# Kernel optimization log

Hardware: AMD Instinct MI355X
Metric: run time of the kernel (lower is better)

## Reference

```python
import jax, jax.numpy as jnp
import numpy as np

_JPEG_QUANT_TABLE = np.array([
    [16, 11, 10, 16, 24, 40, 51, 61],
    [12, 12, 14, 19, 26, 58, 60, 55],
    [14, 13, 16, 24, 40, 57, 69, 56],
    [14, 17, 22, 29, 51, 87, 80, 62],
    [18, 22, 37, 56, 68, 109, 103, 77],
    [24, 35, 55, 64, 81, 104, 113, 92],
    [49, 64, 78, 87, 103, 121, 120, 101],
    [72, 92, 95, 98, 112, 100, 103, 99]], dtype=np.float32)


def _dct_matrix():
    # Orthonormal 8x8 DCT-II basis: D[k, i] = alpha(k) * cos(pi*(2i+1)k/16)
    n = 8
    k = np.arange(n)[:, None].astype(np.float64)
    i = np.arange(n)[None, :].astype(np.float64)
    alpha = np.where(k == 0, np.sqrt(1.0 / n), np.sqrt(2.0 / n))
    return jnp.asarray(alpha * np.cos(np.pi * (2 * i + 1) * k / (2 * n)), dtype=jnp.float32)


def setup_inputs() -> dict:
    key = jax.random.key(0)
    image = jax.random.uniform(key, (32, 3, 512, 512), dtype=jnp.float32)
    return {"image": image, "quality": 75}


def reference(image, quality):
    B, C, H, W = image.shape  # H, W divisible by 8 (no padding branch needed)
    bh, bw = H // 8, W // 8

    # libjpeg quality -> scale (quality is a static Python int)
    scale = 5000.0 / quality if quality < 50 else 200.0 - 2.0 * quality
    qtable = jnp.clip(jnp.asarray(_JPEG_QUANT_TABLE) * scale / 100.0, 1.0, 255.0)
    dct = _dct_matrix()

    x = image - 0.5
    # blockify: (B,C,H,W) -> (B*C, bh, bw, 8, 8)
    blocks = x.reshape(B * C, bh, 8, bw, 8).transpose(0, 1, 3, 2, 4)

    # 2D DCT: dct @ block @ dct^T
    dct_blocks = jnp.einsum('ki,...ij,lj->...kl', dct, blocks, dct)

    # quantize with straight-through estimator (forward: round, backward: identity)
    normalized = dct_blocks / qtable
    quantized = normalized + jax.lax.stop_gradient(jnp.round(normalized) - normalized)
    dequantized = quantized * qtable

    # 2D IDCT: dct^T @ block @ dct
    spatial = jnp.einsum('ki,...kl,lj->...ij', dct, dequantized, dct)

    # deblockify: (B*C, bh, bw, 8, 8) -> (B, C, H, W)
    result = spatial.transpose(0, 1, 3, 2, 4).reshape(B, C, H, W)
    return jnp.clip(result + 0.5, 0.0, 1.0)
```

## Files before the change

### kernel.cpp

```cpp
#include <hip/hip_runtime.h>


typedef float v4f __attribute__((ext_vector_type(4)));

static __device__ __constant__ float c_qbase[64] = {
    16.f, 11.f, 10.f, 16.f, 24.f, 40.f, 51.f, 61.f,
    12.f, 12.f, 14.f, 19.f, 26.f, 58.f, 60.f, 55.f,
    14.f, 13.f, 16.f, 24.f, 40.f, 57.f, 69.f, 56.f,
    14.f, 17.f, 22.f, 29.f, 51.f, 87.f, 80.f, 62.f,
    18.f, 22.f, 37.f, 56.f, 68.f, 109.f, 103.f, 77.f,
    24.f, 35.f, 55.f, 64.f, 81.f, 104.f, 113.f, 92.f,
    49.f, 64.f, 78.f, 87.f, 103.f, 121.f, 120.f, 101.f,
    72.f, 92.f, 95.f, 98.f, 112.f, 100.f, 103.f, 99.f
};

#define LDS_PITCH 9

__global__ __launch_bounds__(256, 8)
void jpeg_row_kernel(const float* __restrict__ in, const int* __restrict__ qual,
                     float* __restrict__ out) {
    constexpr float CE[4][4] = {
        { 0.3535533906f,  0.3535533906f,  0.3535533906f,  0.3535533906f },
        { 0.4619397663f,  0.1913417162f, -0.1913417162f, -0.4619397663f },
        { 0.3535533906f, -0.3535533906f, -0.3535533906f,  0.3535533906f },
        { 0.1913417162f, -0.4619397663f,  0.4619397663f, -0.1913417162f }
    };
    constexpr float CO[4][4] = {
        { 0.4903926402f,  0.4157348062f,  0.2777851165f,  0.0975451610f },
        { 0.4157348062f, -0.0975451610f, -0.4903926402f, -0.2777851165f },
        { 0.2777851165f, -0.4903926402f,  0.0975451610f,  0.4157348062f },
        { 0.0975451610f, -0.2777851165f,  0.4157348062f, -0.4903926402f }
    };

    __shared__ float2 qlds[64];
    __shared__ float tr[256 * LDS_PITCH];

    const int tid = threadIdx.x;

    {
        int q = qual[0];
        double sd = (q < 50) ? (5000.0 / (double)q) : (200.0 - 2.0 * (double)q);
        float scale = (float)sd;
        int e = tid & 63;
        float v = c_qbase[e] * scale / 100.0f;
        v = fminf(fmaxf(v, 1.0f), 255.0f);
        qlds[e] = make_float2(v, 1.0f / v);
    }

    const int gt  = blockIdx.x * 256 + tid;
    const int b   = gt >> 3;
    const int r   = gt & 7;
    const int img = b >> 12;
    const int by  = (b >> 6) & 63;
    const int bx  = b & 63;
    const long rowaddr = (((long)img * 512 + (long)by * 8 + r) * 512) + (long)bx * 8;

    float x[8];
    {
        const float4 a  = *reinterpret_cast<const float4*>(in + rowaddr);
        const float4 b4 = *reinterpret_cast<const float4*>(in + rowaddr + 4);
        x[0] = a.x - 0.5f; x[1] = a.y - 0.5f; x[2] = a.z - 0.5f; x[3] = a.w - 0.5f;
        x[4] = b4.x - 0.5f; x[5] = b4.y - 0.5f; x[6] = b4.z - 0.5f; x[7] = b4.w - 0.5f;
    }

    float qk[8], rqk[8];
#pragma unroll
    for (int k = 0; k < 8; ++k) {
        float2 t2 = qlds[k * 8 + r];
        qk[k] = t2.x; rqk[k] = t2.y;
    }

    float u[8];
    {
        float e[4], o[4];
#pragma unroll
        for (int j = 0; j < 4; ++j) { e[j] = x[j] + x[7 - j]; o[j] = x[j] - x[7 - j]; }
#pragma unroll
        for (int m = 0; m < 4; ++m) {
            float se = 0.0f, so = 0.0f;
#pragma unroll
            for (int j = 0; j < 4; ++j) {
                se = fmaf(e[j], CE[m][j], se);
                so = fmaf(o[j], CO[m][j], so);
            }
            u[2 * m] = se; u[2 * m + 1] = so;
        }
    }

    const int base_w = tid * LDS_PITCH;
    const int base_r = (tid & ~7) * LDS_PITCH;
#pragma unroll
    for (int j = 0; j < 8; ++j) tr[base_w + j] = u[j];
    float t[8];
#pragma unroll
    for (int j = 0; j < 8; ++j) t[j] = tr[base_r + j * LDS_PITCH + r];

    float y[8];
    {
        float e[4], o[4];
#pragma unroll
        for (int j = 0; j < 4; ++j) { e[j] = t[j] + t[7 - j]; o[j] = t[j] - t[7 - j]; }
#pragma unroll
        for (int m = 0; m < 4; ++m) {
            float se = 0.0f, so = 0.0f;
#pragma unroll
            for (int j = 0; j < 4; ++j) {
                se = fmaf(e[j], CE[m][j], se);
                so = fmaf(o[j], CO[m][j], so);
            }
            y[2 * m]     = rintf(se * rqk[2 * m])     * qk[2 * m];
            y[2 * m + 1] = rintf(so * rqk[2 * m + 1]) * qk[2 * m + 1];
        }
    }

    float v[8];
#pragma unroll
    for (int j = 0; j < 4; ++j) {
        float a = 0.0f, bb = 0.0f;
#pragma unroll
        for (int m = 0; m < 4; ++m) {
            a  = fmaf(y[2 * m],     CE[m][j], a);
            bb = fmaf(y[2 * m + 1], CO[m][j], bb);
        }
        v[j] = a + bb; v[7 - j] = a - bb;
    }

#pragma unroll
    for (int j = 0; j < 8; ++j) tr[base_w + j] = v[j];
    float w[8];
#pragma unroll
    for (int j = 0; j < 8; ++j) w[j] = tr[base_r + j * LDS_PITCH + r];

    float srow[8];
#pragma unroll
    for (int j = 0; j < 4; ++j) {
        float a = 0.0f, bb = 0.0f;
#pragma unroll
        for (int m = 0; m < 4; ++m) {
            a  = fmaf(w[2 * m],     CE[m][j], a);
            bb = fmaf(w[2 * m + 1], CO[m][j], bb);
        }
        float s0 = a + bb + 0.5f;
        float s1 = a - bb + 0.5f;
        srow[j]     = fminf(fmaxf(s0, 0.0f), 1.0f);
        srow[7 - j] = fminf(fmaxf(s1, 0.0f), 1.0f);
    }
    *reinterpret_cast<float4*>(out + rowaddr)     = make_float4(srow[0], srow[1], srow[2], srow[3]);
    *reinterpret_cast<float4*>(out + rowaddr + 4) = make_float4(srow[4], srow[5], srow[6], srow[7]);
}

extern "C" void kernel_launch(void* const* d_in, const int* in_sizes, int n_in,
                              void* d_out, int out_size, void* d_ws, size_t ws_size,
                              hipStream_t stream) {
    const float* img  = (const float*)d_in[0];
    const int*   qual = (const int*)d_in[1];
    float*       out  = (float*)d_out;

    const int nthreads_total = (out_size / 64) * 8;
    const int block = 256;
    const int grid = nthreads_total / block;

    jpeg_row_kernel<<<grid, block, 0, stream>>>(img, qual, out);
}
```

Before: 38.69 us.

## Process six image planes per thread with register-prefetched loads

Each thread now loops over six 8-pixel rows spaced sixteen image planes apart, so the grid shrinks to a fixed 2048 blocks. The next row's global loads are issued before the current row's DCT/quantize/IDCT, overlapping memory latency with compute and amortizing the quant-table setup. LDS transpose writes are widened to 128-bit vector stores. The fixed grid and NITER hard-code the 96-plane 512x512 input shape, and the vector LDS stores at pitch 9 are only 4-byte aligned for odd thread indices.

```diff
diff --git a/kernel.cpp b/kernel.cpp
--- a/kernel.cpp
+++ b/kernel.cpp
@@ -15,10 +15,11 @@
 };
 
 #define LDS_PITCH 9
+#define NITER 6
 
 __global__ __launch_bounds__(256, 8)
-void jpeg_row_kernel(const float* __restrict__ in, const int* __restrict__ qual,
-                     float* __restrict__ out) {
+void jpeg_persist_kernel(const float* __restrict__ in, const int* __restrict__ qual,
+                         float* __restrict__ out) {
     constexpr float CE[4][4] = {
         { 0.3535533906f,  0.3535533906f,  0.3535533906f,  0.3535533906f },
         { 0.4619397663f,  0.1913417162f, -0.1913417162f, -0.4619397663f },
@@ -53,15 +54,8 @@
     const int img = b >> 12;
     const int by  = (b >> 6) & 63;
     const int bx  = b & 63;
-    const long rowaddr = (((long)img * 512 + (long)by * 8 + r) * 512) + (long)bx * 8;
-
-    float x[8];
-    {
-        const float4 a  = *reinterpret_cast<const float4*>(in + rowaddr);
-        const float4 b4 = *reinterpret_cast<const float4*>(in + rowaddr + 4);
-        x[0] = a.x - 0.5f; x[1] = a.y - 0.5f; x[2] = a.z - 0.5f; x[3] = a.w - 0.5f;
-        x[4] = b4.x - 0.5f; x[5] = b4.y - 0.5f; x[6] = b4.z - 0.5f; x[7] = b4.w - 0.5f;
-    }
+    long addr = (((long)img * 512 + (long)by * 8 + r) * 512) + (long)bx * 8;
+    const long step = 16L * 512 * 512;
 
     float qk[8], rqk[8];
 #pragma unroll
@@ -70,83 +64,100 @@
         qk[k] = t2.x; rqk[k] = t2.y;
     }
 
-    float u[8];
-    {
-        float e[4], o[4];
-#pragma unroll
-        for (int j = 0; j < 4; ++j) { e[j] = x[j] + x[7 - j]; o[j] = x[j] - x[7 - j]; }
-#pragma unroll
-        for (int m = 0; m < 4; ++m) {
-            float se = 0.0f, so = 0.0f;
-#pragma unroll
-            for (int j = 0; j < 4; ++j) {
-                se = fmaf(e[j], CE[m][j], se);
-                so = fmaf(o[j], CO[m][j], so);
-            }
-            u[2 * m] = se; u[2 * m + 1] = so;
-        }
-    }
-
     const int base_w = tid * LDS_PITCH;
     const int base_r = (tid & ~7) * LDS_PITCH;
-#pragma unroll
-    for (int j = 0; j < 8; ++j) tr[base_w + j] = u[j];
-    float t[8];
-#pragma unroll
-    for (int j = 0; j < 8; ++j) t[j] = tr[base_r + j * LDS_PITCH + r];
 
-    float y[8];
-    {
-        float e[4], o[4];
-#pragma unroll
-        for (int j = 0; j < 4; ++j) { e[j] = t[j] + t[7 - j]; o[j] = t[j] - t[7 - j]; }
-#pragma unroll
-        for (int m = 0; m < 4; ++m) {
-            float se = 0.0f, so = 0.0f;
-#pragma unroll
-            for (int j = 0; j < 4; ++j) {
-                se = fmaf(e[j], CE[m][j], se);
-                so = fmaf(o[j], CO[m][j], so);
-            }
-            y[2 * m]     = rintf(se * rqk[2 * m])     * qk[2 * m];
-            y[2 * m + 1] = rintf(so * rqk[2 * m + 1]) * qk[2 * m + 1];
-        }
-    }
-
-    float v[8];
-#pragma unroll
-    for (int j = 0; j < 4; ++j) {
-        float a = 0.0f, bb = 0.0f;
-#pragma unroll
-        for (int m = 0; m < 4; ++m) {
-            a  = fmaf(y[2 * m],     CE[m][j], a);
-            bb = fmaf(y[2 * m + 1], CO[m][j], bb);
-        }
-        v[j] = a + bb; v[7 - j] = a - bb;
-    }
+    float4 a  = *reinterpret_cast<const float4*>(in + addr);
+    float4 b4 = *reinterpret_cast<const float4*>(in + addr + 4);
 
 #pragma unroll
-    for (int j = 0; j < 8; ++j) tr[base_w + j] = v[j];
-    float w[8];
+    for (int it = 0; it < NITER; ++it) {
+        float x[8];
+        x[0] = a.x - 0.5f; x[1] = a.y - 0.5f; x[2] = a.z - 0.5f; x[3] = a.w - 0.5f;
+        x[4] = b4.x - 0.5f; x[5] = b4.y - 0.5f; x[6] = b4.z - 0.5f; x[7] = b4.w - 0.5f;
+        if (it + 1 < NITER) {
+            a  = *reinterpret_cast<const float4*>(in + addr + step);
+            b4 = *reinterpret_cast<const float4*>(in + addr + step + 4);
+        }
+
+        float u[8];
+        {
+            float e[4], o[4];
 #pragma unroll
-    for (int j = 0; j < 8; ++j) w[j] = tr[base_r + j * LDS_PITCH + r];
+            for (int j = 0; j < 4; ++j) { e[j] = x[j] + x[7 - j]; o[j] = x[j] - x[7 - j]; }
+#pragma unroll
+            for (int m = 0; m < 4; ++m) {
+                float se = 0.0f, so = 0.0f;
+#pragma unroll
+                for (int j = 0; j < 4; ++j) {
+                    se = fmaf(e[j], CE[m][j], se);
+                    so = fmaf(o[j], CO[m][j], so);
+                }
+                u[2 * m] = se; u[2 * m + 1] = so;
+            }
+        }
 
-    float srow[8];
+        *reinterpret_cast<v4f*>(&tr[base_w])     = *reinterpret_cast<v4f*>(&u[0]);
+        *reinterpret_cast<v4f*>(&tr[base_w + 4]) = *reinterpret_cast<v4f*>(&u[4]);
+        float t[8];
 #pragma unroll
-    for (int j = 0; j < 4; ++j) {
-        float a = 0.0f, bb = 0.0f;
+        for (int j = 0; j < 8; ++j) t[j] = tr[base_r + j * LDS_PITCH + r];
+
+        float y[8];
+        {
+            float e[4], o[4];
 #pragma unroll
-        for (int m = 0; m < 4; ++m) {
-            a  = fmaf(w[2 * m],     CE[m][j], a);
-            bb = fmaf(w[2 * m + 1], CO[m][j], bb);
+            for (int j = 0; j < 4; ++j) { e[j] = t[j] + t[7 - j]; o[j] = t[j] - t[7 - j]; }
+#pragma unroll
+            for (int m = 0; m < 4; ++m) {
+                float se = 0.0f, so = 0.0f;
+#pragma unroll
+                for (int j = 0; j < 4; ++j) {
+                    se = fmaf(e[j], CE[m][j], se);
+                    so = fmaf(o[j], CO[m][j], so);
+                }
+                y[2 * m]     = rintf(se * rqk[2 * m])     * qk[2 * m];
+                y[2 * m + 1] = rintf(so * rqk[2 * m + 1]) * qk[2 * m + 1];
+            }
         }
-        float s0 = a + bb + 0.5f;
-        float s1 = a - bb + 0.5f;
-        srow[j]     = fminf(fmaxf(s0, 0.0f), 1.0f);
-        srow[7 - j] = fminf(fmaxf(s1, 0.0f), 1.0f);
+
+        float v[8];
+#pragma unroll
+        for (int j = 0; j < 4; ++j) {
+            float sa = 0.0f, sb = 0.0f;
+#pragma unroll
+            for (int m = 0; m < 4; ++m) {
+                sa = fmaf(y[2 * m],     CE[m][j], sa);
+                sb = fmaf(y[2 * m + 1], CO[m][j], sb);
+            }
+            v[j] = sa + sb; v[7 - j] = sa - sb;
+        }
+
+        *reinterpret_cast<v4f*>(&tr[base_w])     = *reinterpret_cast<v4f*>(&v[0]);
+        *reinterpret_cast<v4f*>(&tr[base_w + 4]) = *reinterpret_cast<v4f*>(&v[4]);
+        float w[8];
+#pragma unroll
+        for (int j = 0; j < 8; ++j) w[j] = tr[base_r + j * LDS_PITCH + r];
+
+        float srow[8];
+#pragma unroll
+        for (int j = 0; j < 4; ++j) {
+            float sa = 0.0f, sb = 0.0f;
+#pragma unroll
+            for (int m = 0; m < 4; ++m) {
+                sa = fmaf(w[2 * m],     CE[m][j], sa);
+                sb = fmaf(w[2 * m + 1], CO[m][j], sb);
+            }
+            float s0 = sa + sb + 0.5f;
+            float s1 = sa - sb + 0.5f;
+            srow[j]     = fminf(fmaxf(s0, 0.0f), 1.0f);
+            srow[7 - j] = fminf(fmaxf(s1, 0.0f), 1.0f);
+        }
+        *reinterpret_cast<float4*>(out + addr)     = make_float4(srow[0], srow[1], srow[2], srow[3]);
+        *reinterpret_cast<float4*>(out + addr + 4) = make_float4(srow[4], srow[5], srow[6], srow[7]);
+
+        addr += step;
     }
-    *reinterpret_cast<float4*>(out + rowaddr)     = make_float4(srow[0], srow[1], srow[2], srow[3]);
-    *reinterpret_cast<float4*>(out + rowaddr + 4) = make_float4(srow[4], srow[5], srow[6], srow[7]);
 }
 
 extern "C" void kernel_launch(void* const* d_in, const int* in_sizes, int n_in,
@@ -156,9 +167,6 @@
     const int*   qual = (const int*)d_in[1];
     float*       out  = (float*)d_out;
 
-    const int nthreads_total = (out_size / 64) * 8;
-    const int block = 256;
-    const int grid = nthreads_total / block;
-
-    jpeg_row_kernel<<<grid, block, 0, stream>>>(img, qual, out);
+    const int grid = 2048;
+    jpeg_persist_kernel<<<grid, 256, 0, stream>>>(img, qual, out);
 }
```

Result: faster. 35.86 us (-7.3%).

## Split DCT rows across lane pairs with DPP butterflies and persistent multi-image loop

Applied to the files above, without the earlier changes.

Each 8-pixel row is now handled by two lanes, each holding four values. The even/odd butterflies use DPP lane-xor swaps instead of in-thread adds, which halves the per-thread register arrays and the LDS transpose footprint. The grid is fixed at 2048 blocks, and each thread loops over 12 image slices with a software-prefetched next load, so memory latency overlaps compute. The risks are that the grid size and iteration count are hard-coded to the input shape, and that the extra DPP and sign-select operations add instructions per element.

```diff
diff --git a/kernel.cpp b/kernel.cpp
--- a/kernel.cpp
+++ b/kernel.cpp
@@ -1,7 +1,5 @@
 #include <hip/hip_runtime.h>
 
-
-typedef float v4f __attribute__((ext_vector_type(4)));
 
 static __device__ __constant__ float c_qbase[64] = {
     16.f, 11.f, 10.f, 16.f, 24.f, 40.f, 51.f, 61.f,
@@ -14,11 +12,17 @@
     72.f, 92.f, 95.f, 98.f, 112.f, 100.f, 103.f, 99.f
 };
 
-#define LDS_PITCH 9
+#define NITER 12
+
+__device__ __forceinline__ float lane_xor1(float v) {
+    int i = __builtin_bit_cast(int, v);
+    i = __builtin_amdgcn_update_dpp(i, i, 0xB1, 0xF, 0xF, false);
+    return __builtin_bit_cast(float, i);
+}
 
 __global__ __launch_bounds__(256, 8)
-void jpeg_row_kernel(const float* __restrict__ in, const int* __restrict__ qual,
-                     float* __restrict__ out) {
+void jpeg_half_kernel(const float* __restrict__ in, const int* __restrict__ qual,
+                      float* __restrict__ out) {
     constexpr float CE[4][4] = {
         { 0.3535533906f,  0.3535533906f,  0.3535533906f,  0.3535533906f },
         { 0.4619397663f,  0.1913417162f, -0.1913417162f, -0.4619397663f },
@@ -33,7 +37,7 @@
     };
 
     __shared__ float2 qlds[64];
-    __shared__ float tr[256 * LDS_PITCH];
+    __shared__ float tr[4 * 288];
 
     const int tid = threadIdx.x;
 
@@ -47,106 +51,118 @@
         qlds[e] = make_float2(v, 1.0f / v);
     }
 
-    const int gt  = blockIdx.x * 256 + tid;
-    const int b   = gt >> 3;
-    const int r   = gt & 7;
-    const int img = b >> 12;
-    const int by  = (b >> 6) & 63;
-    const int bx  = b & 63;
-    const long rowaddr = (((long)img * 512 + (long)by * 8 + r) * 512) + (long)bx * 8;
+    const int wave = tid >> 6;
+    const int t    = tid & 63;
+    const int h    = t & 1;
+    const int B    = (t >> 1) & 3;
+    const int rc   = t >> 3;
+    const float sgn  = h ? -1.0f : 1.0f;
+    const float msgn = -sgn;
 
-    float x[8];
-    {
-        const float4 a  = *reinterpret_cast<const float4*>(in + rowaddr);
-        const float4 b4 = *reinterpret_cast<const float4*>(in + rowaddr + 4);
-        x[0] = a.x - 0.5f; x[1] = a.y - 0.5f; x[2] = a.z - 0.5f; x[3] = a.w - 0.5f;
-        x[4] = b4.x - 0.5f; x[5] = b4.y - 0.5f; x[6] = b4.z - 0.5f; x[7] = b4.w - 0.5f;
+    float CM[4][4];
+#pragma unroll
+    for (int m = 0; m < 4; ++m)
+#pragma unroll
+        for (int i = 0; i < 4; ++i)
+            CM[m][i] = h ? -CO[m][3 - i] : CE[m][i];
+
+    float q4[4], rq4[4];
+#pragma unroll
+    for (int m = 0; m < 4; ++m) {
+        float2 p = qlds[(2 * m + h) * 8 + rc];
+        q4[m] = p.x; rq4[m] = p.y;
     }
 
-    float qk[8], rqk[8];
+    const int wB    = wave * 288 + B * 72;
+    const int baseA = wB + rc * 9 + h;
+    const int baseB = wB + 36 * h + rc;
+
+    const int blk = (blockIdx.x * 4 + wave) * 4 + B;
+    const int img = blk >> 12;
+    const int by  = (blk >> 6) & 63;
+    const int bx  = blk & 63;
+    long addr = ((long)(img * 512 + by * 8 + rc)) * 512 + bx * 8 + h * 4;
+    const long step = 8L * 512 * 512;
+
+    float4 ld = *reinterpret_cast<const float4*>(in + addr);
+
 #pragma unroll
-    for (int k = 0; k < 8; ++k) {
-        float2 t2 = qlds[k * 8 + r];
-        qk[k] = t2.x; rqk[k] = t2.y;
-    }
+    for (int it = 0; it < NITER; ++it) {
+        float xm[4] = { ld.x - 0.5f, ld.y - 0.5f, ld.z - 0.5f, ld.w - 0.5f };
+        if (it + 1 < NITER)
+            ld = *reinterpret_cast<const float4*>(in + addr + step);
 
-    float u[8];
-    {
-        float e[4], o[4];
+        float rex[4], g[4], u[4];
 #pragma unroll
-        for (int j = 0; j < 4; ++j) { e[j] = x[j] + x[7 - j]; o[j] = x[j] - x[7 - j]; }
+        for (int i = 0; i < 4; ++i) rex[i] = lane_xor1(xm[i]);
+#pragma unroll
+        for (int i = 0; i < 4; ++i) g[i] = fmaf(sgn, rex[3 - i], xm[i]);
 #pragma unroll
         for (int m = 0; m < 4; ++m) {
-            float se = 0.0f, so = 0.0f;
+            float s = 0.0f;
 #pragma unroll
-            for (int j = 0; j < 4; ++j) {
-                se = fmaf(e[j], CE[m][j], se);
-                so = fmaf(o[j], CO[m][j], so);
-            }
-            u[2 * m] = se; u[2 * m + 1] = so;
+            for (int i = 0; i < 4; ++i) s = fmaf(g[i], CM[m][i], s);
+            u[m] = s;
         }
-    }
 
-    const int base_w = tid * LDS_PITCH;
-    const int base_r = (tid & ~7) * LDS_PITCH;
 #pragma unroll
-    for (int j = 0; j < 8; ++j) tr[base_w + j] = u[j];
-    float t[8];
+        for (int m = 0; m < 4; ++m) tr[baseA + 2 * m] = u[m];
+        float t4[4];
 #pragma unroll
-    for (int j = 0; j < 8; ++j) t[j] = tr[base_r + j * LDS_PITCH + r];
+        for (int j = 0; j < 4; ++j) t4[j] = tr[baseB + 9 * j];
 
-    float y[8];
-    {
-        float e[4], o[4];
 #pragma unroll
-        for (int j = 0; j < 4; ++j) { e[j] = t[j] + t[7 - j]; o[j] = t[j] - t[7 - j]; }
+        for (int j = 0; j < 4; ++j) rex[j] = lane_xor1(t4[j]);
+#pragma unroll
+        for (int j = 0; j < 4; ++j) g[j] = fmaf(sgn, rex[3 - j], t4[j]);
+        float yq[4];
 #pragma unroll
         for (int m = 0; m < 4; ++m) {
-            float se = 0.0f, so = 0.0f;
+            float s = 0.0f;
 #pragma unroll
-            for (int j = 0; j < 4; ++j) {
-                se = fmaf(e[j], CE[m][j], se);
-                so = fmaf(o[j], CO[m][j], so);
-            }
-            y[2 * m]     = rintf(se * rqk[2 * m])     * qk[2 * m];
-            y[2 * m + 1] = rintf(so * rqk[2 * m + 1]) * qk[2 * m + 1];
+            for (int j = 0; j < 4; ++j) s = fmaf(g[j], CM[m][j], s);
+            yq[m] = rintf(s * rq4[m]) * q4[m];
         }
-    }
 
-    float v[8];
+        float pjt[4], vr[4];
 #pragma unroll
-    for (int j = 0; j < 4; ++j) {
-        float a = 0.0f, bb = 0.0f;
+        for (int j = 0; j < 4; ++j) {
+            float s = 0.0f;
 #pragma unroll
-        for (int m = 0; m < 4; ++m) {
-            a  = fmaf(y[2 * m],     CE[m][j], a);
-            bb = fmaf(y[2 * m + 1], CO[m][j], bb);
+            for (int m = 0; m < 4; ++m) s = fmaf(yq[m], CM[m][j], s);
+            pjt[j] = s;
         }
-        v[j] = a + bb; v[7 - j] = a - bb;
-    }
+#pragma unroll
+        for (int j = 0; j < 4; ++j) rex[j] = lane_xor1(pjt[j]);
+#pragma unroll
+        for (int j = 0; j < 4; ++j) vr[j] = fmaf(msgn, rex[3 - j], pjt[j]);
 
 #pragma unroll
-    for (int j = 0; j < 8; ++j) tr[base_w + j] = v[j];
-    float w[8];
+        for (int j = 0; j < 4; ++j) tr[baseB + 9 * j] = vr[j];
+        float w4[4];
 #pragma unroll
-    for (int j = 0; j < 8; ++j) w[j] = tr[base_r + j * LDS_PITCH + r];
+        for (int m = 0; m < 4; ++m) w4[m] = tr[baseA + 2 * m];
 
-    float srow[8];
+        float p2[4], px[4];
 #pragma unroll
-    for (int j = 0; j < 4; ++j) {
-        float a = 0.0f, bb = 0.0f;
+        for (int d = 0; d < 4; ++d) {
+            float s = 0.0f;
 #pragma unroll
-        for (int m = 0; m < 4; ++m) {
-            a  = fmaf(w[2 * m],     CE[m][j], a);
-            bb = fmaf(w[2 * m + 1], CO[m][j], bb);
+            for (int m = 0; m < 4; ++m) s = fmaf(w4[m], CM[m][d], s);
+            p2[d] = s;
         }
-        float s0 = a + bb + 0.5f;
-        float s1 = a - bb + 0.5f;
-        srow[j]     = fminf(fmaxf(s0, 0.0f), 1.0f);
-        srow[7 - j] = fminf(fmaxf(s1, 0.0f), 1.0f);
+#pragma unroll
+        for (int d = 0; d < 4; ++d) px[d] = lane_xor1(p2[d]);
+        float F[4];
+#pragma unroll
+        for (int d = 0; d < 4; ++d) {
+            float s = fmaf(msgn, px[3 - d], p2[d]) + 0.5f;
+            F[d] = fminf(fmaxf(s, 0.0f), 1.0f);
+        }
+
+        *reinterpret_cast<float4*>(out + addr) = make_float4(F[0], F[1], F[2], F[3]);
+        addr += step;
     }
-    *reinterpret_cast<float4*>(out + rowaddr)     = make_float4(srow[0], srow[1], srow[2], srow[3]);
-    *reinterpret_cast<float4*>(out + rowaddr + 4) = make_float4(srow[4], srow[5], srow[6], srow[7]);
 }
 
 extern "C" void kernel_launch(void* const* d_in, const int* in_sizes, int n_in,
@@ -156,9 +172,5 @@
     const int*   qual = (const int*)d_in[1];
     float*       out  = (float*)d_out;
 
-    const int nthreads_total = (out_size / 64) * 8;
-    const int block = 256;
-    const int grid = nthreads_total / block;
-
-    jpeg_row_kernel<<<grid, block, 0, stream>>>(img, qual, out);
+    jpeg_half_kernel<<<2048, 256, 0, stream>>>(img, qual, out);
 }
```

Measured after the change: 35.82 us, median of 2. 7.4% less time.
